# Performance work log

Measured on AMD Instinct MI355X. Metric: run time of the kernel, lower is better.

## Reference

```python
import jax, jax.numpy as jnp
import numpy as np

N = 50000      # nodes
E = 800000     # edges (avg degree 16)
H = 2          # heads
IN = 128       # in_channels
OUT = 32       # out_channels


def setup_inputs() -> dict:
    key = jax.random.key(0)
    k1, k2, k3, k4, k5, k6 = jax.random.split(key, 6)
    x = jax.random.normal(k1, (N, IN), jnp.float32)
    pos = jax.random.normal(k2, (N, 3), jnp.float32)
    # xavier-ish scaled params
    W = jax.random.normal(k3, (H, IN, OUT), jnp.float32) * (1.0 / np.sqrt(IN))
    attn = jax.random.normal(k4, (H, 2 * OUT), jnp.float32) * (1.0 / np.sqrt(2 * OUT))
    row = jax.random.randint(k5, (E,), 0, N, dtype=jnp.int32)
    col = jax.random.randint(k6, (E,), 0, N, dtype=jnp.int32)
    return {"x": x, "pos": pos, "W": W, "attn": attn, "row": row, "col": col}


def _segment_softmax(logits, seg, n):
    # numerically-stable softmax grouped by destination node `seg`
    m = jax.ops.segment_max(logits, seg, num_segments=n)
    m = jnp.where(jnp.isfinite(m), m, 0.0)          # empty segments -> 0
    z = jnp.exp(logits - m[seg])
    s = jax.ops.segment_sum(z, seg, num_segments=n)
    return z / jnp.maximum(s[seg], 1e-16)


def reference(x, pos, W, attn, row, col):
    n = x.shape[0]
    out = jnp.einsum('ni,hio->hno', x, W)           # [H,N,h] per-head projection
    # add self loops (num_nodes), PyG fills self-loop edge weight with 1
    loop = jnp.arange(n, dtype=row.dtype)
    row2 = jnp.concatenate([row, loop])             # [E'] = E + N
    col2 = jnp.concatenate([col, loop])
    d = jnp.sqrt(jnp.sum((pos[col] - pos[row]) ** 2, axis=-1))   # [E]
    dist = jnp.maximum(jnp.concatenate([d, jnp.ones(n, x.dtype)]), 1e-6)  # [E']
    src = out[:, row2]                              # edge gather  [H,E',h]
    e = jnp.concatenate([src, src], axis=-1)        # duplicated src (per source) [H,E',2h]
    logits = jnp.einsum('hed,hd->he', e, attn)      # per-edge attention score [H,E']
    alpha = jax.vmap(lambda l: _segment_softmax(l, row2, n))(logits)  # [H,E']
    s = e.sum(axis=-1) * alpha / dist               # weighted per-edge scalar [H,E']
    node = jax.vmap(lambda v: jax.ops.segment_sum(v, row2, num_segments=n))(s)  # [H,N]
    return node[:, row2] - node[:, col2]            # indexed subtraction [H,E']
```

## Files before the change

kernel.cpp:

```cpp
#include <hip/hip_runtime.h>

#define IN_DIM 128
#define OUT_DIM 32
#define NHEAD 2
#define BINSZ 12500
#define NSTRIPE 64
#define EB_THREADS 1024
#define FIX 4.0f
#define CNT_SHIFT 25


__device__ __forceinline__ void edge_accum(int r, int c, int base, int lim,
                                           const float* __restrict__ pos,
                                           unsigned* __restrict__ acc) {
    int rb = r - base;
    if ((unsigned)rb < (unsigned)lim) {
        float dx = pos[c * 3 + 0] - pos[r * 3 + 0];
        float dy = pos[c * 3 + 1] - pos[r * 3 + 1];
        float dz = pos[c * 3 + 2] - pos[r * 3 + 2];
        float inv = 1.0f / fmaxf(sqrtf(dx * dx + dy * dy + dz * dz), 1e-6f);
        atomicAdd(&acc[rb], (1u << CNT_SHIFT) + (unsigned)(inv * FIX + 0.5f));
    }
}

__global__ __launch_bounds__(EB_THREADS) void k_edges(
        const int* __restrict__ row, const int* __restrict__ col,
        const float* __restrict__ pos, unsigned* __restrict__ partial,
        int N, int E, int nbins) {
    __shared__ unsigned acc[BINSZ];
    int bin = blockIdx.x % nbins;
    int s   = blockIdx.x / nbins;
    int base = bin * BINSZ;
    int lim  = min(BINSZ, N - base);
    for (int j = threadIdx.x; j < BINSZ; j += EB_THREADS) acc[j] = 0u;
    __syncthreads();

    int slen = (E + NSTRIPE - 1) / NSTRIPE;
    int e0 = s * slen;
    int e1 = min(e0 + slen, E);
    if ((e0 & 3) == 0) {
        for (int e = e0 + (int)threadIdx.x * 4; e < e1; e += EB_THREADS * 4) {
            if (e + 3 < e1) {
                int4 r4 = *(const int4*)(row + e);
                int4 c4 = *(const int4*)(col + e);
                edge_accum(r4.x, c4.x, base, lim, pos, acc);
                edge_accum(r4.y, c4.y, base, lim, pos, acc);
                edge_accum(r4.z, c4.z, base, lim, pos, acc);
                edge_accum(r4.w, c4.w, base, lim, pos, acc);
            } else {
                for (int k = e; k < e1; ++k)
                    edge_accum(row[k], col[k], base, lim, pos, acc);
            }
        }
    } else {
        for (int e = e0 + (int)threadIdx.x; e < e1; e += EB_THREADS)
            edge_accum(row[e], col[e], base, lim, pos, acc);
    }

    __syncthreads();
    unsigned* dst = partial + (size_t)s * N + base;
    for (int j = threadIdx.x; j < lim; j += EB_THREADS) dst[j] = acc[j];
}

__global__ void k_factor(const unsigned* __restrict__ partial,
                         const float* __restrict__ W,
                         float* __restrict__ fac, float* __restrict__ wsum, int N) {
    int i = blockIdx.x * blockDim.x + threadIdx.x;
    if (blockIdx.x == 0 && threadIdx.x < NHEAD * IN_DIM) {
        const float4* wp = (const float4*)(W + threadIdx.x * OUT_DIM);
        float4 a = wp[0], b = wp[1], c = wp[2], d = wp[3];
        float4 e = wp[4], f = wp[5], g = wp[6], h = wp[7];
        wsum[threadIdx.x] = ((a.x+a.y+a.z+a.w) + (b.x+b.y+b.z+b.w))
                          + ((c.x+c.y+c.z+c.w) + (d.x+d.y+d.z+d.w))
                          + ((e.x+e.y+e.z+e.w) + (f.x+f.y+f.z+f.w))
                          + ((g.x+g.y+g.z+g.w) + (h.x+h.y+h.z+h.w));
    }
    if (i >= N) return;
    unsigned v = 0;
    #pragma unroll 8
    for (int s = 0; s < NSTRIPE; ++s) v += partial[(size_t)s * N + i];
    float invsum = (float)(v & ((1u << CNT_SHIFT) - 1)) * (1.0f / FIX);
    float cnt = 1.0f + (float)(v >> CNT_SHIFT);
    fac[i] = 2.0f * (1.0f + invsum) / cnt;
}

__global__ void k_node(const float* __restrict__ x, const float* __restrict__ wsum,
                       const float* __restrict__ fac,
                       float2* __restrict__ node2, int N) {
    int gid = blockIdx.x * blockDim.x + threadIdx.x;
    int i = gid >> 4;
    int lid = gid & 15;
    if (i >= N) return;
    const float4* xp = (const float4*)(x + (long)i * IN_DIM);
    const float4* w0 = (const float4*)(wsum);
    const float4* w1 = (const float4*)(wsum + IN_DIM);
    float s0 = 0.f, s1 = 0.f;
    #pragma unroll
    for (int q = 0; q < 2; ++q) {
        int idx = lid * 2 + q;
        float4 xv = xp[idx];
        float4 a = w0[idx];
        float4 b = w1[idx];
        s0 += xv.x * a.x + xv.y * a.y + xv.z * a.z + xv.w * a.w;
        s1 += xv.x * b.x + xv.y * b.y + xv.z * b.z + xv.w * b.w;
    }
    #pragma unroll
    for (int off = 8; off >= 1; off >>= 1) {
        s0 += __shfl_xor(s0, off, 16);
        s1 += __shfl_xor(s1, off, 16);
    }
    if (lid == 0) {
        float fc = fac[i];
        node2[i] = make_float2(s0 * fc, s1 * fc);
    }
}

__global__ void k_out(const int* __restrict__ row, const int* __restrict__ col,
                      const float2* __restrict__ node2,
                      float* __restrict__ out, int E, int M) {
    int k = blockIdx.x * blockDim.x + threadIdx.x;
    if (k >= M) return;
    float o0 = 0.f, o1 = 0.f;
    if (k < E) {
        float2 nr = node2[row[k]];
        float2 nc = node2[col[k]];
        o0 = nr.x - nc.x;
        o1 = nr.y - nc.y;
    }
    out[k]     = o0;
    out[M + k] = o1;
}

extern "C" void kernel_launch(void* const* d_in, const int* in_sizes, int n_in,
                              void* d_out, int out_size, void* d_ws, size_t ws_size,
                              hipStream_t stream) {
    const float* x   = (const float*)d_in[0];
    const float* pos = (const float*)d_in[1];
    const float* W   = (const float*)d_in[2];
    const int* row = (const int*)d_in[4];
    const int* col = (const int*)d_in[5];
    float* out = (float*)d_out;

    const int N = in_sizes[0] / IN_DIM;
    const int E = in_sizes[4];
    const int M = E + N;
    const int nbins = (N + BINSZ - 1) / BINSZ;

    unsigned* partial = (unsigned*)d_ws;
    float* rest = (float*)(partial + (size_t)NSTRIPE * N);
    float* fac  = rest;
    float* wsum = rest + N;
    float2* node2 = (float2*)(rest + N + 256 + ((N + 256) & 1));

    const int b = 256;
    k_edges <<<nbins * NSTRIPE, EB_THREADS, 0, stream>>>(row, col, pos, partial, N, E, nbins);
    k_factor<<<(N + b - 1) / b,      b, 0, stream>>>(partial, W, fac, wsum, N);
    k_node  <<<(N * 16 + b - 1) / b, b, 0, stream>>>(x, wsum, fac, node2, N);
    k_out   <<<(M + b - 1) / b,      b, 0, stream>>>(row, col, node2, out, E, M);
}
```

Before: 40.26 us.

## Fuse edge binning with node projection, compress partials to u16, vectorize output

Merges the edge-accumulation and node-projection work into one launch, with extra blocks computing per-node x·wsum while the edge blocks fill LDS bins. Per-stripe partials are packed into 16-bit words (3-bit count, 13-bit fixed-point inverse distance), with a float atomic fallback for large inverse distances. This halves partial traffic in the fold, and the fold now also applies the factor. The output kernel handles two edges per thread. Clamping counts and sums to the 16-bit fields can lose precision or saturate, and an extra memset launch is added.

```diff
diff --git a/kernel.cpp b/kernel.cpp
--- a/kernel.cpp
+++ b/kernel.cpp
@@ -5,125 +5,155 @@
 #define NHEAD 2
 #define BINSZ 12500
 #define NSTRIPE 64
-#define EB_THREADS 1024
-#define FIX 4.0f
-#define CNT_SHIFT 25
+#define THREADS 1024
+#define PBLOCKS 256
+#define FIX 32.0f
+#define INV_FALLBACK 128.0f
+#define LDS_CNT_SHIFT 25
+#define U16_INV_MASK 0x1FFFu
+#define U16_CNT_SHIFT 13
 
+__global__ __launch_bounds__(THREADS) void k_main(
+        const int* __restrict__ row, const int* __restrict__ col,
+        const float* __restrict__ pos, const float* __restrict__ x,
+        const float* __restrict__ W,
+        unsigned short* __restrict__ partial, float* __restrict__ Dbig,
+        float2* __restrict__ S2, int N, int E, int nbins, int eblocks) {
+    __shared__ __align__(16) unsigned acc[BINSZ];
+    const int b = blockIdx.x;
+    if (b < eblocks) {
+        const int bin  = b % nbins;
+        const int s    = b / nbins;
+        const int base = bin * BINSZ;
+        const int lim  = min(BINSZ, N - base);
+        for (int j = threadIdx.x; j < BINSZ; j += THREADS) acc[j] = 0u;
+        __syncthreads();
 
-__device__ __forceinline__ void edge_accum(int r, int c, int base, int lim,
-                                           const float* __restrict__ pos,
-                                           unsigned* __restrict__ acc) {
-    int rb = r - base;
-    if ((unsigned)rb < (unsigned)lim) {
-        float dx = pos[c * 3 + 0] - pos[r * 3 + 0];
-        float dy = pos[c * 3 + 1] - pos[r * 3 + 1];
-        float dz = pos[c * 3 + 2] - pos[r * 3 + 2];
-        float inv = 1.0f / fmaxf(sqrtf(dx * dx + dy * dy + dz * dz), 1e-6f);
-        atomicAdd(&acc[rb], (1u << CNT_SHIFT) + (unsigned)(inv * FIX + 0.5f));
+        const int slen = (E + NSTRIPE - 1) / NSTRIPE;
+        const int e0 = s * slen;
+        const int e1 = min(e0 + slen, E);
+
+        auto accum = [&](int r, int c) {
+            int rb = r - base;
+            if ((unsigned)rb < (unsigned)lim) {
+                float dx = pos[c * 3 + 0] - pos[r * 3 + 0];
+                float dy = pos[c * 3 + 1] - pos[r * 3 + 1];
+                float dz = pos[c * 3 + 2] - pos[r * 3 + 2];
+                float inv = 1.0f / fmaxf(sqrtf(dx * dx + dy * dy + dz * dz), 1e-6f);
+                if (inv <= INV_FALLBACK) {
+                    atomicAdd(&acc[rb], (1u << LDS_CNT_SHIFT) + (unsigned)(inv * FIX + 0.5f));
+                } else {
+                    atomicAdd(&acc[rb], 1u << LDS_CNT_SHIFT);
+                    atomicAdd(&Dbig[r], inv);
+                }
+            }
+        };
+
+        if (((e0 | e1) & 3) == 0) {
+            for (int e = e0 + (int)threadIdx.x * 4; e < e1; e += THREADS * 4) {
+                int4 r4 = *(const int4*)(row + e);
+                int4 c4 = *(const int4*)(col + e);
+                accum(r4.x, c4.x); accum(r4.y, c4.y);
+                accum(r4.z, c4.z); accum(r4.w, c4.w);
+            }
+        } else {
+            for (int e = e0 + (int)threadIdx.x; e < e1; e += THREADS)
+                accum(row[e], col[e]);
+        }
+
+        __syncthreads();
+        unsigned short* dst = partial + (size_t)s * N + base;
+        for (int j = threadIdx.x; j < lim; j += THREADS) {
+            unsigned v   = acc[j];
+            unsigned cnt = v >> LDS_CNT_SHIFT;
+            unsigned inv = v & ((1u << LDS_CNT_SHIFT) - 1u);
+            cnt = min(cnt, 7u);
+            inv = min(inv, U16_INV_MASK);
+            dst[j] = (unsigned short)((cnt << U16_CNT_SHIFT) | inv);
+        }
+    } else {
+        float* wl = (float*)acc;
+        if (threadIdx.x < NHEAD * IN_DIM) {
+            const float4* wp = (const float4*)(W + threadIdx.x * OUT_DIM);
+            float s = 0.f;
+            #pragma unroll
+            for (int q = 0; q < 8; ++q) {
+                float4 v = wp[q];
+                s += (v.x + v.y) + (v.z + v.w);
+            }
+            wl[threadIdx.x] = s;
+        }
+        __syncthreads();
+
+        const int lid = threadIdx.x & 15;
+        const float4* wv = (const float4*)wl;
+        float4 w0a = wv[lid * 2],      w0b = wv[lid * 2 + 1];
+        float4 w1a = wv[32 + lid * 2], w1b = wv[32 + lid * 2 + 1];
+
+        const int g      = (b - eblocks) * (THREADS / 16) + (threadIdx.x >> 4);
+        const int stride = (gridDim.x - eblocks) * (THREADS / 16);
+        for (int i = g; i < N; i += stride) {
+            const float4* xp = (const float4*)(x + (size_t)i * IN_DIM);
+            float4 xa = xp[lid * 2], xb = xp[lid * 2 + 1];
+            float s0 = (xa.x * w0a.x + xa.y * w0a.y + xa.z * w0a.z + xa.w * w0a.w)
+                     + (xb.x * w0b.x + xb.y * w0b.y + xb.z * w0b.z + xb.w * w0b.w);
+            float s1 = (xa.x * w1a.x + xa.y * w1a.y + xa.z * w1a.z + xa.w * w1a.w)
+                     + (xb.x * w1b.x + xb.y * w1b.y + xb.z * w1b.z + xb.w * w1b.w);
+            #pragma unroll
+            for (int off = 8; off >= 1; off >>= 1) {
+                s0 += __shfl_xor(s0, off, 16);
+                s1 += __shfl_xor(s1, off, 16);
+            }
+            if (lid == 0) S2[i] = make_float2(s0, s1);
+        }
     }
 }
 
-__global__ __launch_bounds__(EB_THREADS) void k_edges(
-        const int* __restrict__ row, const int* __restrict__ col,
-        const float* __restrict__ pos, unsigned* __restrict__ partial,
-        int N, int E, int nbins) {
-    __shared__ unsigned acc[BINSZ];
-    int bin = blockIdx.x % nbins;
-    int s   = blockIdx.x / nbins;
-    int base = bin * BINSZ;
-    int lim  = min(BINSZ, N - base);
-    for (int j = threadIdx.x; j < BINSZ; j += EB_THREADS) acc[j] = 0u;
-    __syncthreads();
-
-    int slen = (E + NSTRIPE - 1) / NSTRIPE;
-    int e0 = s * slen;
-    int e1 = min(e0 + slen, E);
-    if ((e0 & 3) == 0) {
-        for (int e = e0 + (int)threadIdx.x * 4; e < e1; e += EB_THREADS * 4) {
-            if (e + 3 < e1) {
-                int4 r4 = *(const int4*)(row + e);
-                int4 c4 = *(const int4*)(col + e);
-                edge_accum(r4.x, c4.x, base, lim, pos, acc);
-                edge_accum(r4.y, c4.y, base, lim, pos, acc);
-                edge_accum(r4.z, c4.z, base, lim, pos, acc);
-                edge_accum(r4.w, c4.w, base, lim, pos, acc);
-            } else {
-                for (int k = e; k < e1; ++k)
-                    edge_accum(row[k], col[k], base, lim, pos, acc);
-            }
-        }
-    } else {
-        for (int e = e0 + (int)threadIdx.x; e < e1; e += EB_THREADS)
-            edge_accum(row[e], col[e], base, lim, pos, acc);
+__global__ void k_fold(const unsigned short* __restrict__ partial,
+                       const float* __restrict__ Dbig,
+                       const float2* __restrict__ S2,
+                       float2* __restrict__ node2, int N) {
+    int i = blockIdx.x * blockDim.x + threadIdx.x;
+    if (i >= N) return;
+    unsigned isum = 0, csum = 0;
+    #pragma unroll 16
+    for (int s = 0; s < NSTRIPE; ++s) {
+        unsigned v = partial[(size_t)s * N + i];
+        isum += v & U16_INV_MASK;
+        csum += v >> U16_CNT_SHIFT;
     }
-
-    __syncthreads();
-    unsigned* dst = partial + (size_t)s * N + base;
-    for (int j = threadIdx.x; j < lim; j += EB_THREADS) dst[j] = acc[j];
+    float invsum = (float)isum * (1.0f / FIX) + Dbig[i];
+    float fac = 2.0f * (1.0f + invsum) / (1.0f + (float)csum);
+    float2 sv = S2[i];
+    node2[i] = make_float2(sv.x * fac, sv.y * fac);
 }
 
-__global__ void k_factor(const unsigned* __restrict__ partial,
-                         const float* __restrict__ W,
-                         float* __restrict__ fac, float* __restrict__ wsum, int N) {
-    int i = blockIdx.x * blockDim.x + threadIdx.x;
-    if (blockIdx.x == 0 && threadIdx.x < NHEAD * IN_DIM) {
-        const float4* wp = (const float4*)(W + threadIdx.x * OUT_DIM);
-        float4 a = wp[0], b = wp[1], c = wp[2], d = wp[3];
-        float4 e = wp[4], f = wp[5], g = wp[6], h = wp[7];
-        wsum[threadIdx.x] = ((a.x+a.y+a.z+a.w) + (b.x+b.y+b.z+b.w))
-                          + ((c.x+c.y+c.z+c.w) + (d.x+d.y+d.z+d.w))
-                          + ((e.x+e.y+e.z+e.w) + (f.x+f.y+f.z+f.w))
-                          + ((g.x+g.y+g.z+g.w) + (h.x+h.y+h.z+h.w));
+__global__ void k_out2(const int* __restrict__ row, const int* __restrict__ col,
+                       const float2* __restrict__ node2,
+                       float* __restrict__ out, int E, int M) {
+    int k = (blockIdx.x * blockDim.x + threadIdx.x) * 2;
+    if (k >= M) return;
+    float2 a = make_float2(0.f, 0.f), b = make_float2(0.f, 0.f);
+    if (k < E) {
+        int2 r2 = *(const int2*)(row + k);
+        int2 c2 = *(const int2*)(col + k);
+        float2 nr0 = node2[r2.x], nc0 = node2[c2.x];
+        float2 nr1 = node2[r2.y], nc1 = node2[c2.y];
+        a = make_float2(nr0.x - nc0.x, nr1.x - nc1.x);
+        b = make_float2(nr0.y - nc0.y, nr1.y - nc1.y);
     }
-    if (i >= N) return;
-    unsigned v = 0;
-    #pragma unroll 8
-    for (int s = 0; s < NSTRIPE; ++s) v += partial[(size_t)s * N + i];
-    float invsum = (float)(v & ((1u << CNT_SHIFT) - 1)) * (1.0f / FIX);
-    float cnt = 1.0f + (float)(v >> CNT_SHIFT);
-    fac[i] = 2.0f * (1.0f + invsum) / cnt;
+    *(float2*)(out + k)     = a;
+    *(float2*)(out + M + k) = b;
 }
 
-__global__ void k_node(const float* __restrict__ x, const float* __restrict__ wsum,
-                       const float* __restrict__ fac,
-                       float2* __restrict__ node2, int N) {
-    int gid = blockIdx.x * blockDim.x + threadIdx.x;
-    int i = gid >> 4;
-    int lid = gid & 15;
-    if (i >= N) return;
-    const float4* xp = (const float4*)(x + (long)i * IN_DIM);
-    const float4* w0 = (const float4*)(wsum);
-    const float4* w1 = (const float4*)(wsum + IN_DIM);
-    float s0 = 0.f, s1 = 0.f;
-    #pragma unroll
-    for (int q = 0; q < 2; ++q) {
-        int idx = lid * 2 + q;
-        float4 xv = xp[idx];
-        float4 a = w0[idx];
-        float4 b = w1[idx];
-        s0 += xv.x * a.x + xv.y * a.y + xv.z * a.z + xv.w * a.w;
-        s1 += xv.x * b.x + xv.y * b.y + xv.z * b.z + xv.w * b.w;
-    }
-    #pragma unroll
-    for (int off = 8; off >= 1; off >>= 1) {
-        s0 += __shfl_xor(s0, off, 16);
-        s1 += __shfl_xor(s1, off, 16);
-    }
-    if (lid == 0) {
-        float fc = fac[i];
-        node2[i] = make_float2(s0 * fc, s1 * fc);
-    }
-}
-
-__global__ void k_out(const int* __restrict__ row, const int* __restrict__ col,
-                      const float2* __restrict__ node2,
-                      float* __restrict__ out, int E, int M) {
+__global__ void k_out1(const int* __restrict__ row, const int* __restrict__ col,
+                       const float2* __restrict__ node2,
+                       float* __restrict__ out, int E, int M) {
     int k = blockIdx.x * blockDim.x + threadIdx.x;
     if (k >= M) return;
     float o0 = 0.f, o1 = 0.f;
     if (k < E) {
-        float2 nr = node2[row[k]];
-        float2 nc = node2[col[k]];
+        float2 nr = node2[row[k]], nc = node2[col[k]];
         o0 = nr.x - nc.x;
         o1 = nr.y - nc.y;
     }
@@ -145,16 +175,20 @@
     const int E = in_sizes[4];
     const int M = E + N;
     const int nbins = (N + BINSZ - 1) / BINSZ;
+    const int eblocks = nbins * NSTRIPE;
 
-    unsigned* partial = (unsigned*)d_ws;
-    float* rest = (float*)(partial + (size_t)NSTRIPE * N);
-    float* fac  = rest;
-    float* wsum = rest + N;
-    float2* node2 = (float2*)(rest + N + 256 + ((N + 256) & 1));
+    float2* S2    = (float2*)d_ws;
+    float2* node2 = S2 + N;
+    float*  Dbig  = (float*)(node2 + N);
+    unsigned short* partial = (unsigned short*)(Dbig + N);
 
-    const int b = 256;
-    k_edges <<<nbins * NSTRIPE, EB_THREADS, 0, stream>>>(row, col, pos, partial, N, E, nbins);
-    k_factor<<<(N + b - 1) / b,      b, 0, stream>>>(partial, W, fac, wsum, N);
-    k_node  <<<(N * 16 + b - 1) / b, b, 0, stream>>>(x, wsum, fac, node2, N);
-    k_out   <<<(M + b - 1) / b,      b, 0, stream>>>(row, col, node2, out, E, M);
+    hipMemsetAsync(Dbig, 0, (size_t)N * sizeof(float), stream);
+
+    k_main<<<eblocks + PBLOCKS, THREADS, 0, stream>>>(
+        row, col, pos, x, W, partial, Dbig, S2, N, E, nbins, eblocks);
+    k_fold<<<(N + 255) / 256, 256, 0, stream>>>(partial, Dbig, S2, node2, N);
+    if (((E | M) & 1) == 0)
+        k_out2<<<((M >> 1) + 255) / 256, 256, 0, stream>>>(row, col, node2, out, E, M);
+    else
+        k_out1<<<(M + 255) / 256, 256, 0, stream>>>(row, col, node2, out, E, M);
 }
```

Result: no change. 40.67 us (+1.0%).
